# Performance work log

Hardware: AMD Instinct MI355X
Metric: run time of the kernel (lower is better)

Reference implementation:

```python
import jax, jax.numpy as jnp
import numpy as np

T_THRESHOLD = 1e-4      # VolumeRenderer T_threshold / composite_test_fw threshold
NEAR_DISTANCE = 0.01    # hparams.NEAR_DISTANCE clamp applied to hits_t


def setup_inputs() -> dict:
    key = jax.random.key(0)
    k1, k2, k3 = jax.random.split(key, 3)
    N_rays, N_samples = 65536, 256
    rays = jax.random.normal(k1, (N_rays, 6), dtype=jnp.float32)
    # sigmas are NN outputs (post-activation densities >= 0)
    sigmas = 2.0 * jax.random.uniform(k2, (N_rays, N_samples), dtype=jnp.float32)
    rgbs = jax.random.uniform(k3, (N_rays, N_samples, 3), dtype=jnp.float32)
    center = jnp.zeros((3,), dtype=jnp.float32)
    half_size = jnp.ones((3,), dtype=jnp.float32)
    return {"rays": rays, "sigmas": sigmas, "rgbs": rgbs,
            "center": center, "half_size": half_size}


def reference(rays, sigmas, rgbs, center, half_size):
    N_samples = sigmas.shape[1]
    rays_o = rays[:, 0:3]                      # (R, 3)
    rays_d = rays[:, 3:6]
    rays_d = rays_d / (jnp.linalg.norm(rays_d, axis=-1, keepdims=True) + 1e-8)

    # --- RayAABBIntersector: slab test against the scene box ---
    safe_d = jnp.where(jnp.abs(rays_d) > 1e-8, rays_d, 1e-8)
    inv_d = 1.0 / safe_d
    t1 = (center - half_size - rays_o) * inv_d
    t2 = (center + half_size - rays_o) * inv_d
    tmin = jnp.max(jnp.minimum(t1, t2), axis=-1)   # (R,)
    tmax = jnp.min(jnp.maximum(t1, t2), axis=-1)
    hit = tmax > jnp.maximum(tmin, 0.0)
    near = jnp.maximum(tmin, 0.0)
    # forward(): clamp near bound below NEAR_DISTANCE
    near = jnp.where(hit & (near < NEAR_DISTANCE), NEAR_DISTANCE, near)
    far = jnp.where(hit, tmax, near)

    # --- RayMarcher: uniform marching between near/far (padded, masked) ---
    delta = (far - near) / N_samples                               # (R,)
    offs = (jnp.arange(N_samples, dtype=jnp.float32) + 0.5)
    ts = near[:, None] + offs[None, :] * delta[:, None]            # (R, S)

    # --- VolumeRenderer: front-to-back compositing with T_threshold stop ---
    sd = sigmas * delta[:, None]                                   # sigma * dt
    # exclusive transmittance: T_i = exp(-sum_{j<i} sigma_j dt_j)
    T = jnp.exp(-(jnp.cumsum(sd, axis=1) - sd))
    alpha = 1.0 - jnp.exp(-sd)
    alive = (T >= T_THRESHOLD) & hit[:, None]
    ws = jnp.where(alive, alpha * T, 0.0)                          # (R, S)

    opacity = jnp.sum(ws, axis=1)                                  # (R,)
    rgb = jnp.einsum('rs,rsc->rc', ws, rgbs)                       # (R, 3)
    # exp_step_factor != 0 (aabb > 0.5) -> black background
    rgb_bg = jnp.zeros((3,), dtype=rgb.dtype)
    rgb = rgb + rgb_bg * (1.0 - opacity)[:, None]
    return rgb
```

## Files before the change

kernel.cpp:

```cpp
#include <hip/hip_runtime.h>
#include <math.h>

#define N_RAYS 65536
#define N_SAMPLES 256
#define T_THRESHOLD 1e-4f
#define NEAR_DISTANCE 0.01f

template <int CTRL, int ROW_MASK>
__device__ __forceinline__ float dpp_add(float v) {
    int iv = __builtin_bit_cast(int, v);
    int sh = __builtin_amdgcn_update_dpp(0, iv, CTRL, ROW_MASK, 0xf, false);
    return v + __builtin_bit_cast(float, sh);
}

__device__ __forceinline__ float wave_incl_scan(float x) {
    x = dpp_add<0x111, 0xf>(x);
    x = dpp_add<0x112, 0xf>(x);
    x = dpp_add<0x114, 0xf>(x);
    x = dpp_add<0x118, 0xf>(x);
    x = dpp_add<0x142, 0xa>(x);
    x = dpp_add<0x143, 0xc>(x);
    return x;
}

__global__ __launch_bounds__(256) void ngp_render_kernel(
    const float* __restrict__ rays,
    const float* __restrict__ sigmas,
    const float* __restrict__ rgbs,
    const float* __restrict__ center,
    const float* __restrict__ half_size,
    float* __restrict__ out)
{
    const int gtid = blockIdx.x * blockDim.x + threadIdx.x;
    const int ray  = gtid >> 6;
    const int lane = threadIdx.x & 63;
    if (ray >= N_RAYS) return;

    const float* rp = rays + (size_t)ray * 6;
    float o[3] = { rp[0], rp[1], rp[2] };
    float d[3] = { rp[3], rp[4], rp[5] };
    float inv_norm = 1.0f / (sqrtf(d[0]*d[0] + d[1]*d[1] + d[2]*d[2]) + 1e-8f);
    d[0] *= inv_norm; d[1] *= inv_norm; d[2] *= inv_norm;

    float tmin = -INFINITY, tmax = INFINITY;
    #pragma unroll
    for (int a = 0; a < 3; ++a) {
        float da  = (fabsf(d[a]) > 1e-8f) ? d[a] : 1e-8f;
        float inv = 1.0f / da;
        float t1  = (center[a] - half_size[a] - o[a]) * inv;
        float t2  = (center[a] + half_size[a] - o[a]) * inv;
        tmin = fmaxf(tmin, fminf(t1, t2));
        tmax = fminf(tmax, fmaxf(t1, t2));
    }
    const bool hit = tmax > fmaxf(tmin, 0.0f);

    if (!hit) {
        if (lane == 0) {
            float* op = out + (size_t)ray * 3;
            op[0] = 0.0f; op[1] = 0.0f; op[2] = 0.0f;
        }
        return;
    }

    float near = fmaxf(tmin, 0.0f);
    if (near < NEAR_DISTANCE) near = NEAR_DISTANCE;
    const float delta = (tmax - near) * (1.0f / (float)N_SAMPLES);

    const float4 sg = *reinterpret_cast<const float4*>(
        sigmas + (size_t)ray * N_SAMPLES + lane * 4);
    const float sd0 = sg.x * delta;
    const float sd1 = sg.y * delta;
    const float sd2 = sg.z * delta;
    const float sd3 = sg.w * delta;
    const float p0 = sd0;
    const float p1 = p0 + sd1;
    const float p2 = p1 + sd2;
    const float p3 = p2 + sd3;

    const float incl = wave_incl_scan(p3);
    const float excl = incl - p3;

    const float T0 = __expf(-excl);
    const float T1 = __expf(-(excl + p0));
    const float T2 = __expf(-(excl + p1));
    const float T3 = __expf(-(excl + p2));
    const float a0 = 1.0f - __expf(-sd0);
    const float a1 = 1.0f - __expf(-sd1);
    const float a2 = 1.0f - __expf(-sd2);
    const float a3 = 1.0f - __expf(-sd3);
    const float ws0 = (T0 >= T_THRESHOLD) ? a0 * T0 : 0.0f;
    const float ws1 = (T1 >= T_THRESHOLD) ? a1 * T1 : 0.0f;
    const float ws2 = (T2 >= T_THRESHOLD) ? a2 * T2 : 0.0f;
    const float ws3 = (T3 >= T_THRESHOLD) ? a3 * T3 : 0.0f;

    const float* rb = rgbs + (size_t)ray * N_SAMPLES * 3 + (size_t)lane * 12;
    const float4 r0 = *reinterpret_cast<const float4*>(rb + 0);
    const float4 r1 = *reinterpret_cast<const float4*>(rb + 4);
    const float4 r2 = *reinterpret_cast<const float4*>(rb + 8);
    float R = ws0 * r0.x + ws1 * r0.w + ws2 * r1.z + ws3 * r2.y;
    float G = ws0 * r0.y + ws1 * r1.x + ws2 * r1.w + ws3 * r2.z;
    float B = ws0 * r0.z + ws1 * r1.y + ws2 * r2.x + ws3 * r2.w;

    R = wave_incl_scan(R);
    G = wave_incl_scan(G);
    B = wave_incl_scan(B);
    if (lane == 63) {
        float* op = out + (size_t)ray * 3;
        op[0] = R; op[1] = G; op[2] = B;
    }
}

extern "C" void kernel_launch(void* const* d_in, const int* in_sizes, int n_in,
                              void* d_out, int out_size, void* d_ws, size_t ws_size,
                              hipStream_t stream) {
    const float* rays      = (const float*)d_in[0];
    const float* sigmas    = (const float*)d_in[1];
    const float* rgbs      = (const float*)d_in[2];
    const float* center    = (const float*)d_in[3];
    const float* half_size = (const float*)d_in[4];
    float* out = (float*)d_out;

    const int threads = 256;
    const int blocks  = N_RAYS / 4;
    ngp_render_kernel<<<blocks, threads, 0, stream>>>(
        rays, sigmas, rgbs, center, half_size, out);
}
```

Measured before the change: 24.90 us.

## Split ray-box setup into per-ray kernel and use transmittance differences for weights

Moves the ray normalization and AABB slab test into a separate one-thread-per-ray kernel that writes per-ray deltas (negative for misses) to workspace. The render kernel then reads a scalar delta instead of having all 64 lanes redo the setup math. The weights are rewritten as T_i - T_{i+1}, which drops four exp calls. The cost is an extra kernel launch and a global round trip for deltas, and the subtraction form can differ slightly in rounding from alpha*T.

```diff
diff --git a/kernel.cpp b/kernel.cpp
--- a/kernel.cpp
+++ b/kernel.cpp
@@ -5,6 +5,7 @@
 #define N_SAMPLES 256
 #define T_THRESHOLD 1e-4f
 #define NEAR_DISTANCE 0.01f
+
 
 template <int CTRL, int ROW_MASK>
 __device__ __forceinline__ float dpp_add(float v) {
@@ -23,17 +24,14 @@
     return x;
 }
 
-__global__ __launch_bounds__(256) void ngp_render_kernel(
+__global__ __launch_bounds__(256) void ngp_setup_kernel(
     const float* __restrict__ rays,
-    const float* __restrict__ sigmas,
-    const float* __restrict__ rgbs,
     const float* __restrict__ center,
     const float* __restrict__ half_size,
+    float* __restrict__ deltas,
     float* __restrict__ out)
 {
-    const int gtid = blockIdx.x * blockDim.x + threadIdx.x;
-    const int ray  = gtid >> 6;
-    const int lane = threadIdx.x & 63;
+    const int ray = blockIdx.x * blockDim.x + threadIdx.x;
     if (ray >= N_RAYS) return;
 
     const float* rp = rays + (size_t)ray * 6;
@@ -54,17 +52,30 @@
     }
     const bool hit = tmax > fmaxf(tmin, 0.0f);
 
-    if (!hit) {
-        if (lane == 0) {
-            float* op = out + (size_t)ray * 3;
-            op[0] = 0.0f; op[1] = 0.0f; op[2] = 0.0f;
-        }
-        return;
+    if (hit) {
+        float near = fmaxf(tmin, 0.0f);
+        if (near < NEAR_DISTANCE) near = NEAR_DISTANCE;
+        deltas[ray] = (tmax - near) * (1.0f / (float)N_SAMPLES);
+    } else {
+        deltas[ray] = -1.0f;
+        float* op = out + (size_t)ray * 3;
+        op[0] = 0.0f; op[1] = 0.0f; op[2] = 0.0f;
     }
+}
 
-    float near = fmaxf(tmin, 0.0f);
-    if (near < NEAR_DISTANCE) near = NEAR_DISTANCE;
-    const float delta = (tmax - near) * (1.0f / (float)N_SAMPLES);
+__global__ __launch_bounds__(256) void ngp_render_kernel(
+    const float* __restrict__ sigmas,
+    const float* __restrict__ rgbs,
+    const float* __restrict__ deltas,
+    float* __restrict__ out)
+{
+    const int lane = threadIdx.x & 63;
+    const int ray  = __builtin_amdgcn_readfirstlane(
+        (blockIdx.x * blockDim.x + threadIdx.x) >> 6);
+    if (ray >= N_RAYS) return;
+
+    const float delta = deltas[ray];
+    if (delta < 0.0f) return;
 
     const float4 sg = *reinterpret_cast<const float4*>(
         sigmas + (size_t)ray * N_SAMPLES + lane * 4);
@@ -84,14 +95,11 @@
     const float T1 = __expf(-(excl + p0));
     const float T2 = __expf(-(excl + p1));
     const float T3 = __expf(-(excl + p2));
-    const float a0 = 1.0f - __expf(-sd0);
-    const float a1 = 1.0f - __expf(-sd1);
-    const float a2 = 1.0f - __expf(-sd2);
-    const float a3 = 1.0f - __expf(-sd3);
-    const float ws0 = (T0 >= T_THRESHOLD) ? a0 * T0 : 0.0f;
-    const float ws1 = (T1 >= T_THRESHOLD) ? a1 * T1 : 0.0f;
-    const float ws2 = (T2 >= T_THRESHOLD) ? a2 * T2 : 0.0f;
-    const float ws3 = (T3 >= T_THRESHOLD) ? a3 * T3 : 0.0f;
+    const float T4 = __expf(-incl);
+    const float ws0 = (T0 >= T_THRESHOLD) ? T0 - T1 : 0.0f;
+    const float ws1 = (T1 >= T_THRESHOLD) ? T1 - T2 : 0.0f;
+    const float ws2 = (T2 >= T_THRESHOLD) ? T2 - T3 : 0.0f;
+    const float ws3 = (T3 >= T_THRESHOLD) ? T3 - T4 : 0.0f;
 
     const float* rb = rgbs + (size_t)ray * N_SAMPLES * 3 + (size_t)lane * 12;
     const float4 r0 = *reinterpret_cast<const float4*>(rb + 0);
@@ -118,10 +126,12 @@
     const float* rgbs      = (const float*)d_in[2];
     const float* center    = (const float*)d_in[3];
     const float* half_size = (const float*)d_in[4];
-    float* out = (float*)d_out;
+    float* out    = (float*)d_out;
+    float* deltas = (float*)d_ws;
 
-    const int threads = 256;
-    const int blocks  = N_RAYS / 4;
-    ngp_render_kernel<<<blocks, threads, 0, stream>>>(
-        rays, sigmas, rgbs, center, half_size, out);
+    ngp_setup_kernel<<<N_RAYS / 256, 256, 0, stream>>>(
+        rays, center, half_size, deltas, out);
+
+    ngp_render_kernel<<<N_RAYS / 4, 256, 0, stream>>>(
+        sigmas, rgbs, deltas, out);
 }
```

Result: slower. 28.79 us (+15.6%).

## Process two rays per wavefront and compute weights as transmittance differences

Applied to the files above, without the earlier changes.

Each wavefront now handles two rays, with 32 lanes per ray and 8 samples per lane, so the scans use one fewer DPP step and the launch uses half as many blocks. Alpha times T is replaced by T_i minus T_{i+1}, which removes the separate exp(-sd) evaluations. Loads are guarded per half-wave so a ray that misses does not fetch data while its partner ray proceeds. The difference form changes floating-point rounding slightly, and the per-lane loads become wider.

```diff
diff --git a/kernel.cpp b/kernel.cpp
--- a/kernel.cpp
+++ b/kernel.cpp
@@ -13,13 +13,12 @@
     return v + __builtin_bit_cast(float, sh);
 }
 
-__device__ __forceinline__ float wave_incl_scan(float x) {
+__device__ __forceinline__ float half_incl_scan(float x) {
     x = dpp_add<0x111, 0xf>(x);
     x = dpp_add<0x112, 0xf>(x);
     x = dpp_add<0x114, 0xf>(x);
     x = dpp_add<0x118, 0xf>(x);
     x = dpp_add<0x142, 0xa>(x);
-    x = dpp_add<0x143, 0xc>(x);
     return x;
 }
 
@@ -31,9 +30,10 @@
     const float* __restrict__ half_size,
     float* __restrict__ out)
 {
-    const int gtid = blockIdx.x * blockDim.x + threadIdx.x;
-    const int ray  = gtid >> 6;
-    const int lane = threadIdx.x & 63;
+    const int lane   = threadIdx.x & 63;
+    const int s      = lane & 31;
+    const int waveId = (blockIdx.x * blockDim.x + threadIdx.x) >> 6;
+    const int ray    = waveId * 2 + (lane >> 5);
     if (ray >= N_RAYS) return;
 
     const float* rp = rays + (size_t)ray * 6;
@@ -54,57 +54,81 @@
     }
     const bool hit = tmax > fmaxf(tmin, 0.0f);
 
-    if (!hit) {
-        if (lane == 0) {
+    if (__ballot(hit) == 0ull) {
+        if (s == 31) {
             float* op = out + (size_t)ray * 3;
             op[0] = 0.0f; op[1] = 0.0f; op[2] = 0.0f;
         }
         return;
     }
 
-    float near = fmaxf(tmin, 0.0f);
-    if (near < NEAR_DISTANCE) near = NEAR_DISTANCE;
-    const float delta = (tmax - near) * (1.0f / (float)N_SAMPLES);
+    float delta = 0.0f;
+    if (hit) {
+        float near = fmaxf(tmin, 0.0f);
+        if (near < NEAR_DISTANCE) near = NEAR_DISTANCE;
+        delta = (tmax - near) * (1.0f / (float)N_SAMPLES);
+    }
 
-    const float4 sg = *reinterpret_cast<const float4*>(
-        sigmas + (size_t)ray * N_SAMPLES + lane * 4);
-    const float sd0 = sg.x * delta;
-    const float sd1 = sg.y * delta;
-    const float sd2 = sg.z * delta;
-    const float sd3 = sg.w * delta;
+    float4 sg0 = make_float4(0,0,0,0), sg1 = make_float4(0,0,0,0);
+    float4 r0 = sg0, r1 = sg0, r2 = sg0, r3 = sg0, r4 = sg0, r5 = sg0;
+    if (hit) {
+        const float* sp = sigmas + (size_t)ray * N_SAMPLES + s * 8;
+        sg0 = *reinterpret_cast<const float4*>(sp);
+        sg1 = *reinterpret_cast<const float4*>(sp + 4);
+        const float* rb = rgbs + (size_t)ray * N_SAMPLES * 3 + (size_t)s * 24;
+        r0 = *reinterpret_cast<const float4*>(rb + 0);
+        r1 = *reinterpret_cast<const float4*>(rb + 4);
+        r2 = *reinterpret_cast<const float4*>(rb + 8);
+        r3 = *reinterpret_cast<const float4*>(rb + 12);
+        r4 = *reinterpret_cast<const float4*>(rb + 16);
+        r5 = *reinterpret_cast<const float4*>(rb + 20);
+    }
+
+    const float sd0 = sg0.x * delta, sd1 = sg0.y * delta;
+    const float sd2 = sg0.z * delta, sd3 = sg0.w * delta;
+    const float sd4 = sg1.x * delta, sd5 = sg1.y * delta;
+    const float sd6 = sg1.z * delta, sd7 = sg1.w * delta;
     const float p0 = sd0;
     const float p1 = p0 + sd1;
     const float p2 = p1 + sd2;
     const float p3 = p2 + sd3;
+    const float p4 = p3 + sd4;
+    const float p5 = p4 + sd5;
+    const float p6 = p5 + sd6;
+    const float p7 = p6 + sd7;
 
-    const float incl = wave_incl_scan(p3);
-    const float excl = incl - p3;
+    const float incl = half_incl_scan(p7);
+    const float excl = incl - p7;
 
     const float T0 = __expf(-excl);
     const float T1 = __expf(-(excl + p0));
     const float T2 = __expf(-(excl + p1));
     const float T3 = __expf(-(excl + p2));
-    const float a0 = 1.0f - __expf(-sd0);
-    const float a1 = 1.0f - __expf(-sd1);
-    const float a2 = 1.0f - __expf(-sd2);
-    const float a3 = 1.0f - __expf(-sd3);
-    const float ws0 = (T0 >= T_THRESHOLD) ? a0 * T0 : 0.0f;
-    const float ws1 = (T1 >= T_THRESHOLD) ? a1 * T1 : 0.0f;
-    const float ws2 = (T2 >= T_THRESHOLD) ? a2 * T2 : 0.0f;
-    const float ws3 = (T3 >= T_THRESHOLD) ? a3 * T3 : 0.0f;
+    const float T4 = __expf(-(excl + p3));
+    const float T5 = __expf(-(excl + p4));
+    const float T6 = __expf(-(excl + p5));
+    const float T7 = __expf(-(excl + p6));
+    const float T8 = __expf(-incl);
+    const float ws0 = (T0 >= T_THRESHOLD) ? T0 - T1 : 0.0f;
+    const float ws1 = (T1 >= T_THRESHOLD) ? T1 - T2 : 0.0f;
+    const float ws2 = (T2 >= T_THRESHOLD) ? T2 - T3 : 0.0f;
+    const float ws3 = (T3 >= T_THRESHOLD) ? T3 - T4 : 0.0f;
+    const float ws4 = (T4 >= T_THRESHOLD) ? T4 - T5 : 0.0f;
+    const float ws5 = (T5 >= T_THRESHOLD) ? T5 - T6 : 0.0f;
+    const float ws6 = (T6 >= T_THRESHOLD) ? T6 - T7 : 0.0f;
+    const float ws7 = (T7 >= T_THRESHOLD) ? T7 - T8 : 0.0f;
 
-    const float* rb = rgbs + (size_t)ray * N_SAMPLES * 3 + (size_t)lane * 12;
-    const float4 r0 = *reinterpret_cast<const float4*>(rb + 0);
-    const float4 r1 = *reinterpret_cast<const float4*>(rb + 4);
-    const float4 r2 = *reinterpret_cast<const float4*>(rb + 8);
-    float R = ws0 * r0.x + ws1 * r0.w + ws2 * r1.z + ws3 * r2.y;
-    float G = ws0 * r0.y + ws1 * r1.x + ws2 * r1.w + ws3 * r2.z;
-    float B = ws0 * r0.z + ws1 * r1.y + ws2 * r2.x + ws3 * r2.w;
+    float R = ws0*r0.x + ws1*r0.w + ws2*r1.z + ws3*r2.y
+            + ws4*r3.x + ws5*r3.w + ws6*r4.z + ws7*r5.y;
+    float G = ws0*r0.y + ws1*r1.x + ws2*r1.w + ws3*r2.z
+            + ws4*r3.y + ws5*r4.x + ws6*r4.w + ws7*r5.z;
+    float B = ws0*r0.z + ws1*r1.y + ws2*r2.x + ws3*r2.w
+            + ws4*r3.z + ws5*r4.y + ws6*r5.x + ws7*r5.w;
 
-    R = wave_incl_scan(R);
-    G = wave_incl_scan(G);
-    B = wave_incl_scan(B);
-    if (lane == 63) {
+    R = half_incl_scan(R);
+    G = half_incl_scan(G);
+    B = half_incl_scan(B);
+    if (s == 31) {
         float* op = out + (size_t)ray * 3;
         op[0] = R; op[1] = G; op[2] = B;
     }
@@ -120,8 +144,7 @@
     const float* half_size = (const float*)d_in[4];
     float* out = (float*)d_out;
 
-    const int threads = 256;
-    const int blocks  = N_RAYS / 4;
-    ngp_render_kernel<<<blocks, threads, 0, stream>>>(
+    const int blocks = N_RAYS / 8;
+    ngp_render_kernel<<<blocks, 256, 0, stream>>>(
         rays, sigmas, rgbs, center, half_size, out);
 }
```

After: 24.54 us. About the same (-1.5%).
